# Kernel tuning notes

Measured on AMD Instinct MI355X. Metric: run time of the kernel, lower is better.

Reference implementation:

```python
import jax, jax.numpy as jnp
import numpy as np

N_NODES = 100000
N_EDGES = 1600000
EPS = 1e-5  # nn.BatchNorm1d default eps


def setup_inputs() -> dict:
    key = jax.random.key(0)
    ks = jax.random.split(key, 6)
    x = jax.random.normal(ks[0], (N_NODES, 11), dtype=jnp.float32)
    edge_index = jax.random.randint(ks[1], (2, N_EDGES), 0, N_NODES, dtype=jnp.int64)
    edge_weight = jax.random.uniform(ks[2], (N_EDGES,), dtype=jnp.float32)
    W1 = jax.random.normal(ks[3], (11, 64), dtype=jnp.float32) * 0.3
    b1 = jnp.zeros((64,), dtype=jnp.float32)
    gamma = jnp.ones((64,), dtype=jnp.float32)
    beta = jnp.zeros((64,), dtype=jnp.float32)
    W2 = jax.random.normal(ks[4], (64, 128), dtype=jnp.float32) * 0.125
    b2 = jnp.zeros((128,), dtype=jnp.float32)
    return {"x": x, "edge_index": edge_index, "edge_weight": edge_weight,
            "W1": W1, "b1": b1, "gamma": gamma, "beta": beta, "W2": W2, "b2": b2}


def _gcn_conv(x, row, col, w, W, b, n_nodes):
    """PyG GCNConv: h = x @ W; symmetric-norm aggregate at col; + bias.
    row/col/w already include self loops (weight 1.0)."""
    h = x @ W  # [N, F_out]
    deg = jax.ops.segment_sum(w, col, num_segments=n_nodes)  # [N]
    dinv = jnp.where(deg > 0, jax.lax.rsqrt(jnp.maximum(deg, 1e-12)), 0.0)
    norm = dinv[row] * w * dinv[col]  # [E+N]
    msg = h[row] * norm[:, None]  # gather + scale, [E+N, F_out]
    out = jax.ops.segment_sum(msg, col, num_segments=n_nodes)  # scatter-add
    return out + b


def _batch_norm(x, gamma, beta):
    # training-mode BatchNorm1d over node dimension, biased variance
    mean = jnp.mean(x, axis=0)
    var = jnp.mean(jnp.square(x - mean), axis=0)
    return (x - mean) * jax.lax.rsqrt(var + EPS) * gamma + beta


def reference(x, edge_index, edge_weight, W1, b1, gamma, beta, W2, b2):
    n = x.shape[0]
    loops = jnp.arange(n, dtype=edge_index.dtype)
    row = jnp.concatenate([edge_index[0], loops])
    col = jnp.concatenate([edge_index[1], loops])
    w = jnp.concatenate([edge_weight, jnp.ones((n,), dtype=edge_weight.dtype)])

    h = _gcn_conv(x, row, col, w, W1, b1, n)
    h = _batch_norm(h, gamma, beta)
    h = jax.nn.relu(h)
    # dropout is identity at inference (deterministic baseline)
    out = _gcn_conv(h, row, col, w, W2, b2, n)
    return out
```

## Files before the change

kernel.cpp:

```cpp
#include <hip/hip_runtime.h>

#define F0 11
#define F1 64
#define F2 128
#define TN2 128

#define CHUNKS 64
#define BPR 12544
#define WPR (BPR / 2)
#define NBKT (CHUNKS * 8 * 4)
#define NN1 64

__device__ __forceinline__ unsigned short f2bf(float v) {
  unsigned u = __float_as_uint(v);
  unsigned r = u + 0x7FFFu + ((u >> 16) & 1u);
  return (unsigned short)(r >> 16);
}
__device__ __forceinline__ float bf2f(unsigned short s) {
  return __uint_as_float(((unsigned)s) << 16);
}
__device__ __forceinline__ float bf2f_lo(unsigned v) { return __uint_as_float(v << 16); }
__device__ __forceinline__ float bf2f_hi(unsigned v) { return __uint_as_float(v & 0xFFFF0000u); }

__global__ void k_pad(const float* __restrict__ x, unsigned short* __restrict__ x16b, int n) {
  int i = blockIdx.x * blockDim.x + threadIdx.x;
  if (i >= n * 16) return;
  int r = i >> 4, f = i & 15;
  x16b[i] = (f < F0) ? f2bf(x[(size_t)r * F0 + f]) : (unsigned short)0;
}

__global__ __launch_bounds__(1024) void k_cnt8(const int* __restrict__ col,
                                               int* __restrict__ bcnt, int E, int CE) {
  __shared__ int scnt[16][8];
  int bid = blockIdx.x;
  int c = bid >> 2, q = bid & 3;
  int e0 = c * CE, e1 = min(E, e0 + CE);
  int S = (CE + 3) >> 2;
  int s0 = e0 + q * S, s1 = min(e1, s0 + S);
  int t = threadIdx.x, wv = t >> 6, lane = t & 63;
  int cr[8] = {0, 0, 0, 0, 0, 0, 0, 0};
  for (int e = s0 + t; e < s1; e += 1024) {
    int r = col[e] / BPR;
#pragma unroll
    for (int rr = 0; rr < 8; rr++) cr[rr] += (r == rr) ? 1 : 0;
  }
#pragma unroll
  for (int rr = 0; rr < 8; rr++) {
    int v = cr[rr];
#pragma unroll
    for (int d = 32; d > 0; d >>= 1) v += __shfl_down(v, d);
    if (lane == 0) scnt[wv][rr] = v;
  }
  __syncthreads();
  if (t < 8) {
    int s = 0;
    for (int i = 0; i < 16; i++) s += scnt[i][t];
    bcnt[(c * 8 + t) * 4 + q] = s;
  }
}

__global__ void k_scan8(const int* __restrict__ bcnt, int* __restrict__ boff) {
  __shared__ int s[1024];
  int t = threadIdx.x;
  int v0 = bcnt[2 * t], v1 = bcnt[2 * t + 1];
  int pv = v0 + v1;
  s[t] = pv;
  __syncthreads();
  for (int d = 1; d < 1024; d <<= 1) {
    int x = (t >= d) ? s[t - d] : 0;
    __syncthreads();
    s[t] += x;
    __syncthreads();
  }
  int ex = s[t] - pv;
  boff[2 * t] = ex;
  boff[2 * t + 1] = ex + v0;
  if (t == 1023) boff[2048] = s[1023];
}

__global__ __launch_bounds__(1024) void k_scatter(const int* __restrict__ col,
                                                  const int* __restrict__ row,
                                                  const float* __restrict__ w,
                                                  const int* __restrict__ boff,
                                                  unsigned short* __restrict__ bloc,
                                                  uint2* __restrict__ brw, int E, int CE) {
  __shared__ int cur[8];
  int bid = blockIdx.x;
  int c = bid >> 2, q = bid & 3;
  int t = threadIdx.x;
  if (t < 8) cur[t] = boff[(c * 8 + t) * 4 + q];
  __syncthreads();
  int e0 = c * CE, e1 = min(E, e0 + CE);
  int S = (CE + 3) >> 2;
  int s0 = e0 + q * S, s1 = min(e1, s0 + S);
  for (int e = s0 + t; e < s1; e += 1024) {
    int b = col[e];
    int r = b / BPR;
    int pos = atomicAdd(&cur[r], 1);
    bloc[pos] = (unsigned short)(b - r * BPR);
    brw[pos] = make_uint2((unsigned)row[e], __float_as_uint(w[e]));
  }
}

__global__ __launch_bounds__(1024) void k_hist2(const unsigned short* __restrict__ bloc,
                                                const int* __restrict__ boff,
                                                unsigned* __restrict__ partial, int ranges) {
  __shared__ unsigned lds[WPR];
  int r = blockIdx.x % ranges;
  int c = blockIdx.x / ranges;
  int t = threadIdx.x;
  for (int i = t; i < WPR; i += 1024) lds[i] = 0;
  __syncthreads();
  int s0 = boff[(c * 8 + r) * 4], s1 = boff[(c * 8 + r) * 4 + 4];
  for (int i = s0 + t; i < s1; i += 1024) {
    int local = bloc[i];
    atomicAdd(&lds[local >> 1], 1u << (16 * (local & 1)));
  }
  __syncthreads();
  unsigned* dst = partial + ((size_t)r * CHUNKS + c) * WPR;
  for (int i = t; i < WPR; i += 1024) dst[i] = lds[i];
}

__global__ void k_colprefix(const unsigned* __restrict__ partial,
                            unsigned short* __restrict__ rel,
                            int* __restrict__ cnt, int N, int npad) {
  int bin = blockIdx.x * blockDim.x + threadIdx.x;
  if (bin >= N) return;
  int r = bin / BPR, local = bin % BPR;
  int word = local >> 1, sh = 16 * (local & 1);
  const unsigned* p = partial + (size_t)r * CHUNKS * WPR + word;
  unsigned acc = 0;
  for (int c = 0; c < CHUNKS; c++) {
    unsigned v = (p[(size_t)c * WPR] >> sh) & 0xFFFFu;
    rel[(size_t)c * npad + bin] = (unsigned short)acc;
    acc += v;
  }
  cnt[bin] = (int)acc;
}

__global__ void k_scan1(const int* __restrict__ cnt, int* __restrict__ offs,
                        int* __restrict__ bsum, int n) {
  __shared__ int s[1024];
  int tid = threadIdx.x;
  int i = blockIdx.x * 1024 + tid;
  int v = (i < n) ? cnt[i] : 0;
  s[tid] = v;
  __syncthreads();
  for (int d = 1; d < 1024; d <<= 1) {
    int t = (tid >= d) ? s[tid - d] : 0;
    __syncthreads();
    s[tid] += t;
    __syncthreads();
  }
  if (i < n) offs[i] = s[tid] - v;
  if (tid == 1023) bsum[blockIdx.x] = s[1023];
}

__global__ void k_scan2(int* __restrict__ bsum, int nb) {
  __shared__ int s[256];
  __shared__ int carry;
  int t = threadIdx.x;
  if (t == 0) carry = 0;
  __syncthreads();
  for (int base = 0; base < nb; base += 256) {
    int v = (base + t < nb) ? bsum[base + t] : 0;
    s[t] = v;
    __syncthreads();
    for (int d = 1; d < 256; d <<= 1) {
      int x = (t >= d) ? s[t - d] : 0;
      __syncthreads();
      s[t] += x;
      __syncthreads();
    }
    int total = s[255];
    if (base + t < nb) bsum[base + t] = carry + s[t] - v;
    __syncthreads();
    if (t == 0) carry += total;
    __syncthreads();
  }
}

__global__ void k_scan3(int* __restrict__ offs, const int* __restrict__ bsum,
                        int n, int total) {
  int i = blockIdx.x * 1024 + threadIdx.x;
  if (i < n) offs[i] += bsum[blockIdx.x];
  if (i == 0) offs[n] = total;
}

__global__ __launch_bounds__(1024) void k_fill2(const unsigned short* __restrict__ bloc,
                                                const uint2* __restrict__ brw,
                                                const int* __restrict__ boff,
                                                const int* __restrict__ offs,
                                                const unsigned short* __restrict__ rel,
                                                uint2* __restrict__ csr8,
                                                int N, int npad, int ranges) {
  __shared__ unsigned cur[WPR];
  int r = blockIdx.x % ranges;
  int c = blockIdx.x / ranges;
  int lo = r * BPR;
  int hi = min(N, lo + BPR);
  int t = threadIdx.x;
  const unsigned* rsrc = (const unsigned*)(rel + (size_t)c * npad + lo);
  int nw = (hi - lo + 1) >> 1;
  for (int i = t; i < nw; i += 1024) cur[i] = rsrc[i];
  __syncthreads();
  int s0 = boff[(c * 8 + r) * 4], s1 = boff[(c * 8 + r) * 4 + 4];
  for (int i = s0 + t; i < s1; i += 1024) {
    int local = bloc[i];
    int sh = 16 * (local & 1);
    unsigned old = atomicAdd(&cur[local >> 1], 1u << sh);
    unsigned myrel = (old >> sh) & 0xFFFFu;
    int pos = offs[lo + local] + (int)myrel;
    uint2 b = brw[i];
    csr8[pos] = make_uint2(b.x | ((unsigned)local << 17), b.y);
  }
}

__global__ void k_deg2(const uint2* __restrict__ csr8, const int* __restrict__ offs,
                       float* __restrict__ dinv, int n) {
  int wid = (blockIdx.x * blockDim.x + threadIdx.x) >> 6;
  int lane = threadIdx.x & 63;
  if (wid >= n) return;
  int s = offs[wid], e = offs[wid + 1];
  float acc = 0.f;
  for (int k = s + lane; k < e; k += 64) acc += __uint_as_float(csr8[k].y);
#pragma unroll
  for (int d = 32; d > 0; d >>= 1) acc += __shfl_down(acc, d);
  if (lane == 0) dinv[wid] = rsqrtf(1.0f + acc);
}

__global__ void k_norm(uint2* __restrict__ csr8, const float* __restrict__ dinv, int E) {
  int i = blockIdx.x * blockDim.x + threadIdx.x;
  if (i >= E) return;
  uint2 v = csr8[i];
  csr8[i].y = __float_as_uint(dinv[v.x & 0x1FFFFu] * __uint_as_float(v.y));
}

__global__ __launch_bounds__(256) void k_agg1e(const unsigned short* __restrict__ x16b,
                                               const int* __restrict__ offs,
                                               const uint2* __restrict__ csr8,
                                               const float* __restrict__ dinv,
                                               const float* __restrict__ W1,
                                               const float* __restrict__ b1,
                                               unsigned short* __restrict__ h,
                                               float2* __restrict__ pbn, int N) {
  __shared__ float Ws[F0 * F1];
  __shared__ float bs[F1];
  __shared__ float sacc[NN1 * 16];
  __shared__ unsigned short sx[NN1 * 16];
  __shared__ float sdinv[NN1];
  __shared__ float sS[4][64], sQ[4][64];
  int t = threadIdx.x;
  int bid = blockIdx.x;
  int n0 = bid * NN1;
  int nn = min(NN1, N - n0);
  int lbase = n0 - (n0 / BPR) * BPR;
  for (int i = t; i < F0 * F1; i += 256) Ws[i] = W1[i];
  if (t < F1) bs[t] = b1[t];
  ((uint2*)sx)[t] = ((const uint2*)(x16b + (size_t)n0 * 16))[t];
  if (t < NN1) sdinv[t] = (t < nn) ? dinv[n0 + t] : 0.f;
  for (int i = t; i < NN1 * 16; i += 256) sacc[i] = 0.f;
  __syncthreads();
  int ebase = offs[n0], eend = offs[n0 + nn];
  int slot = t >> 4, f = t & 15;
  int nsub = (eend - ebase + 15) >> 4;
  int gs = ebase + slot * nsub;
  int ge = min(eend, gs + nsub);
  float sum = 0.f;
  int cid = -1;
  int e = gs;
  for (; e + 4 <= ge; e += 4) {
    uint2 v0 = csr8[e], v1 = csr8[e + 1], v2 = csr8[e + 2], v3 = csr8[e + 3];
    int i0 = (int)(v0.x >> 17) - lbase, i1 = (int)(v1.x >> 17) - lbase;
    int i2 = (int)(v2.x >> 17) - lbase, i3 = (int)(v3.x >> 17) - lbase;
    float c0 = __uint_as_float(v0.y) * bf2f(x16b[(size_t)(v0.x & 0x1FFFFu) * 16 + f]);
    float c1 = __uint_as_float(v1.y) * bf2f(x16b[(size_t)(v1.x & 0x1FFFFu) * 16 + f]);
    float c2 = __uint_as_float(v2.y) * bf2f(x16b[(size_t)(v2.x & 0x1FFFFu) * 16 + f]);
    float c3 = __uint_as_float(v3.y) * bf2f(x16b[(size_t)(v3.x & 0x1FFFFu) * 16 + f]);
    bool sm;
    sm = (i0 == cid); if (!sm && cid >= 0) atomicAdd(&sacc[cid * 16 + f], sum);
    sum = sm ? sum + c0 : c0; cid = i0;
    sm = (i1 == cid); if (!sm) atomicAdd(&sacc[cid * 16 + f], sum);
    sum = sm ? sum + c1 : c1; cid = i1;
    sm = (i2 == cid); if (!sm) atomicAdd(&sacc[cid * 16 + f], sum);
    sum = sm ? sum + c2 : c2; cid = i2;
    sm = (i3 == cid); if (!sm) atomicAdd(&sacc[cid * 16 + f], sum);
    sum = sm ? sum + c3 : c3; cid = i3;
  }
  for (; e < ge; e++) {
    uint2 v0 = csr8[e];
    int i0 = (int)(v0.x >> 17) - lbase;
    float c0 = __uint_as_float(v0.y) * bf2f(x16b[(size_t)(v0.x & 0x1FFFFu) * 16 + f]);
    bool sm = (i0 == cid);
    if (!sm && cid >= 0) atomicAdd(&sacc[cid * 16 + f], sum);
    sum = sm ? sum + c0 : c0; cid = i0;
  }
  if (cid >= 0) atomicAdd(&sacc[cid * 16 + f], sum);
  __syncthreads();
  for (int i = t; i < NN1 * 16; i += 256) {
    float di = sdinv[i >> 4];
    sacc[i] = di * (sacc[i] + di * bf2f(sx[i]));
  }
  __syncthreads();
  int ff = t & 63, wv = t >> 6;
  float S = 0.f, Q = 0.f;
  for (int i = 0; i < 16; i++) {
    int nd = wv + 4 * i;
    if (nd < nn) {
      float o = bs[ff];
#pragma unroll
      for (int k = 0; k < F0; k++) o += sacc[nd * 16 + k] * Ws[k * F1 + ff];
      h[(size_t)(n0 + nd) * F1 + ff] = f2bf(o);
      S += o; Q += o * o;
    }
  }
  sS[wv][ff] = S; sQ[wv][ff] = Q;
  __syncthreads();
  if (t < 64)
    pbn[(size_t)bid * 64 + t] =
        make_float2(sS[0][t] + sS[1][t] + sS[2][t] + sS[3][t],
                    sQ[0][t] + sQ[1][t] + sQ[2][t] + sQ[3][t]);
}

__global__ void k_bn_mid(const float2* __restrict__ pbn, float2* __restrict__ pbn2, int nrows) {
  __shared__ float sS[4][64], sQ[4][64];
  int t = threadIdx.x;
  int f = t & 63, g = t >> 6;
  int rpb = (nrows + 63) / 64;
  int b0 = blockIdx.x * rpb;
  int bend = min(nrows, b0 + rpb);
  float S = 0.f, Q = 0.f;
  for (int b = b0 + g; b < bend; b += 4) {
    float2 v = pbn[(size_t)b * 64 + f];
    S += v.x; Q += v.y;
  }
  sS[g][f] = S; sQ[g][f] = Q;
  __syncthreads();
  if (t < 64)
    pbn2[(size_t)blockIdx.x * 64 + t] =
        make_float2(sS[0][t] + sS[1][t] + sS[2][t] + sS[3][t],
                    sQ[0][t] + sQ[1][t] + sQ[2][t] + sQ[3][t]);
}

__global__ void k_bn_final(const float2* __restrict__ pbn2, const float* __restrict__ gamma,
                           const float* __restrict__ beta, float* __restrict__ scalef,
                           float* __restrict__ shiftf, int n) {
  __shared__ double sS[4][64], sQ[4][64];
  int t = threadIdx.x;
  int f = t & 63, g = t >> 6;
  double S = 0.0, Q = 0.0;
  for (int b = g; b < 64; b += 4) {
    float2 v = pbn2[(size_t)b * 64 + f];
    S += v.x; Q += v.y;
  }
  sS[g][f] = S; sQ[g][f] = Q;
  __syncthreads();
  if (t < 64) {
    double SS = sS[0][t] + sS[1][t] + sS[2][t] + sS[3][t];
    double QQ = sQ[0][t] + sQ[1][t] + sQ[2][t] + sQ[3][t];
    double mean = SS / (double)n;
    double var = QQ / (double)n - mean * mean;
    if (var < 0.0) var = 0.0;
    float scale = gamma[t] * (float)(1.0 / sqrt(var + 1e-5));
    scalef[t] = scale;
    shiftf[t] = beta[t] - (float)mean * scale;
  }
}

__global__ void k_hn(const unsigned short* __restrict__ h, const float* __restrict__ scalef,
                     const float* __restrict__ shiftf, unsigned short* __restrict__ hn,
                     int total4) {
  __shared__ float ssc[64], ssf[64];
  int t = threadIdx.x;
  if (t < 64) { ssc[t] = scalef[t]; ssf[t] = shiftf[t]; }
  __syncthreads();
  int idx = blockIdx.x * blockDim.x + t;
  int stride = gridDim.x * blockDim.x;
  const unsigned long long* hp = (const unsigned long long*)h;
  unsigned long long* hnp = (unsigned long long*)hn;
  for (int i = idx; i < total4; i += stride) {
    unsigned long long vv = hp[i];
    int f0 = (i * 4) & 63;
    float a = fmaxf(fmaf(bf2f_lo((unsigned)vv), ssc[f0 + 0], ssf[f0 + 0]), 0.f);
    float b = fmaxf(fmaf(bf2f_hi((unsigned)vv), ssc[f0 + 1], ssf[f0 + 1]), 0.f);
    float c = fmaxf(fmaf(bf2f_lo((unsigned)(vv >> 32)), ssc[f0 + 2], ssf[f0 + 2]), 0.f);
    float d = fmaxf(fmaf(bf2f_hi((unsigned)(vv >> 32)), ssc[f0 + 3], ssf[f0 + 3]), 0.f);
    hnp[i] = (unsigned long long)f2bf(a) | ((unsigned long long)f2bf(b) << 16) |
             ((unsigned long long)f2bf(c) << 32) | ((unsigned long long)f2bf(d) << 48);
  }
}

__global__ __launch_bounds__(256) void k_agg2e(const unsigned short* __restrict__ hn,
                                               const int* __restrict__ offs,
                                               const uint2* __restrict__ csr8,
                                               const float* __restrict__ dinv,
                                               float* __restrict__ agg2, int N) {
  __shared__ float sacc[NN1 * F1];
  __shared__ float sdinv[NN1];
  int t = threadIdx.x;
  int bid = blockIdx.x;
  int n0 = bid * NN1;
  int nn = min(NN1, N - n0);
  int lbase = n0 - (n0 / BPR) * BPR;
  int lane = t & 63, wv = t >> 6;
  if (t < NN1) sdinv[t] = (t < nn) ? dinv[n0 + t] : 0.f;
  for (int i = t; i < NN1 * F1; i += 256) sacc[i] = 0.f;
  __syncthreads();
  int ebase = offs[n0], eend = offs[n0 + nn];
  int nsub = (eend - ebase + 3) >> 2;
  int gs = ebase + wv * nsub;
  int ge = min(eend, gs + nsub);
  float sum = 0.f;
  int cid = -1;
  int e = gs;
  for (; e + 8 <= ge; e += 8) {
    uint2 v[8];
#pragma unroll
    for (int j = 0; j < 8; j++) v[j] = csr8[e + j];
    float c[8];
    int idx[8];
#pragma unroll
    for (int j = 0; j < 8; j++) {
      idx[j] = (int)(v[j].x >> 17) - lbase;
      c[j] = __uint_as_float(v[j].y) *
             bf2f(hn[(size_t)(v[j].x & 0x1FFFFu) * F1 + lane]);
    }
#pragma unroll
    for (int j = 0; j < 8; j++) {
      bool sm = (idx[j] == cid);
      if (!sm && cid >= 0) atomicAdd(&sacc[cid * F1 + lane], sum);
      sum = sm ? sum + c[j] : c[j];
      cid = idx[j];
    }
  }
  for (; e < ge; e++) {
    uint2 v0 = csr8[e];
    int i0 = (int)(v0.x >> 17) - lbase;
    float c0 = __uint_as_float(v0.y) * bf2f(hn[(size_t)(v0.x & 0x1FFFFu) * F1 + lane]);
    bool sm = (i0 == cid);
    if (!sm && cid >= 0) atomicAdd(&sacc[cid * F1 + lane], sum);
    sum = sm ? sum + c0 : c0;
    cid = i0;
  }
  if (cid >= 0) atomicAdd(&sacc[cid * F1 + lane], sum);
  __syncthreads();
  for (int i = 0; i < 16; i++) {
    int nd = wv + 4 * i;
    if (nd < nn) {
      float di = sdinv[nd];
      float self = bf2f(hn[(size_t)(n0 + nd) * F1 + lane]);
      agg2[(size_t)(n0 + nd) * F1 + lane] = di * (sacc[nd * F1 + lane] + di * self);
    }
  }
}

__global__ __launch_bounds__(256) void k_gemm2(const float* __restrict__ agg2,
                                               const float* __restrict__ W2,
                                               const float* __restrict__ b2,
                                               float* __restrict__ out, int n) {
  __shared__ float Ws[F1 * F2];
  __shared__ float As[F1][TN2];
  int t = threadIdx.x;
  for (int i = t; i < F1 * F2 / 4; i += 256) ((float4*)Ws)[i] = ((const float4*)W2)[i];
  int nb = blockIdx.x * TN2;
  int node = t & 127;
  int kh = (t >> 7) * 32;
  int gnode = nb + node;
  if (gnode < n) {
    const float4* src = (const float4*)(agg2 + (size_t)gnode * F1 + kh);
#pragma unroll
    for (int j = 0; j < 8; j++) {
      float4 v = src[j];
      As[kh + j * 4 + 0][node] = v.x;
      As[kh + j * 4 + 1][node] = v.y;
      As[kh + j * 4 + 2][node] = v.z;
      As[kh + j * 4 + 3][node] = v.w;
    }
  } else {
#pragma unroll
    for (int j = 0; j < 8; j++) {
      As[kh + j * 4 + 0][node] = 0.f;
      As[kh + j * 4 + 1][node] = 0.f;
      As[kh + j * 4 + 2][node] = 0.f;
      As[kh + j * 4 + 3][node] = 0.f;
    }
  }
  __syncthreads();

  int f0 = (t & 15) * 8;
  int n0 = (t >> 4) * 8;
  float acc[8][8];
  float bv[8];
#pragma unroll
  for (int j = 0; j < 8; j++) bv[j] = b2[f0 + j];
#pragma unroll
  for (int i = 0; i < 8; i++)
#pragma unroll
    for (int j = 0; j < 8; j++) acc[i][j] = bv[j];

#pragma unroll 4
  for (int k = 0; k < F1; k++) {
    float4 a0 = *(const float4*)&As[k][n0];
    float4 a1 = *(const float4*)&As[k][n0 + 4];
    float4 w0 = *(const float4*)&Ws[k * F2 + f0];
    float4 w1 = *(const float4*)&Ws[k * F2 + f0 + 4];
    float a[8] = {a0.x, a0.y, a0.z, a0.w, a1.x, a1.y, a1.z, a1.w};
    float w[8] = {w0.x, w0.y, w0.z, w0.w, w1.x, w1.y, w1.z, w1.w};
#pragma unroll
    for (int i = 0; i < 8; i++)
#pragma unroll
      for (int j = 0; j < 8; j++) acc[i][j] += a[i] * w[j];
  }

#pragma unroll
  for (int i = 0; i < 8; i++) {
    int gi = nb + n0 + i;
    if (gi < n) {
      float4 o0 = {acc[i][0], acc[i][1], acc[i][2], acc[i][3]};
      float4 o1 = {acc[i][4], acc[i][5], acc[i][6], acc[i][7]};
      *(float4*)&out[(size_t)gi * F2 + f0] = o0;
      *(float4*)&out[(size_t)gi * F2 + f0 + 4] = o1;
    }
  }
}

extern "C" void kernel_launch(void* const* d_in, const int* in_sizes, int n_in,
                              void* d_out, int out_size, void* d_ws, size_t ws_size,
                              hipStream_t stream) {
  const float* x     = (const float*)d_in[0];
  const int*   ei    = (const int*)d_in[1];
  const float* ew    = (const float*)d_in[2];
  const float* W1    = (const float*)d_in[3];
  const float* b1    = (const float*)d_in[4];
  const float* gamma = (const float*)d_in[5];
  const float* beta  = (const float*)d_in[6];
  const float* W2    = (const float*)d_in[7];
  const float* b2    = (const float*)d_in[8];
  float* out = (float*)d_out;

  int N = in_sizes[0] / F0;
  int E = in_sizes[1] / 2;
  const int* row = ei;
  const int* col = ei + E;
  if (N <= 0) return;

  int CE = (E + CHUNKS - 1) / CHUNKS;
  int RANGES = (N + BPR - 1) / BPR;
  int npad = RANGES * BPR;
  int NBLK = (N + NN1 - 1) / NN1;

  char* p = (char*)d_ws;
  auto alloc = [&](size_t bytes) -> void* {
    void* r = (void*)p;
    p += (bytes + 255) & ~(size_t)255;
    return r;
  };
  size_t partial_bytes = ((size_t)RANGES * CHUNKS * WPR * 4 + 255) & ~(size_t)255;
  size_t rel_bytes     = (size_t)CHUNKS * npad * 2;
  size_t h_bytes       = (size_t)N * F1 * 2;
  size_t region_bytes  = partial_bytes + rel_bytes;
  if (h_bytes > region_bytes) region_bytes = h_bytes;

  float*          dinv    = (float*)alloc((size_t)N * 4);
  int*            cnt     = (int*)alloc((size_t)N * 4);
  int*            offs    = (int*)alloc((size_t)(N + 1) * 4);
  int             NB      = (N + 1023) / 1024;
  int*            bsum    = (int*)alloc((size_t)NB * 4);
  uint2*          csr8    = (uint2*)alloc((size_t)E * 8);
  char*           region  = (char*)alloc(region_bytes);
  unsigned*       partial = (unsigned*)region;
  unsigned short* rel     = (unsigned short*)(region + partial_bytes);
  unsigned short* h       = (unsigned short*)region;
  unsigned short* x16b    = (unsigned short*)alloc((size_t)N * 16 * 2);
  unsigned short* hn      = (unsigned short*)alloc((size_t)N * F1 * 2);
  float*          agg2    = (float*)alloc((size_t)N * F1 * 4);
  float2*         pbn     = (float2*)alloc((size_t)NBLK * 64 * 8);
  float2*         pbn2    = (float2*)alloc((size_t)64 * 64 * 8);
  float*          scalef  = (float*)alloc(64 * 4);
  float*          shiftf  = (float*)alloc(64 * 4);
  int*            bcnt    = (int*)alloc((size_t)NBKT * 4);
  int*            boff    = (int*)alloc((size_t)(NBKT + 1) * 4);
  size_t bloc_bytes = (((size_t)E * 2) + 255) & ~(size_t)255;
  unsigned short* bloc = (unsigned short*)agg2;
  uint2*          brw  = (uint2*)((char*)agg2 + bloc_bytes);
  (void)ws_size; (void)n_in; (void)out_size;

  int bW  = (N + 3) / 4;
  int bG2 = (N + TN2 - 1) / TN2;
  int gRC = CHUNKS * RANGES;

  k_pad<<<(N * 16 + 255) / 256, 256, 0, stream>>>(x, x16b, N);
  k_cnt8<<<CHUNKS * 4, 1024, 0, stream>>>(col, bcnt, E, CE);
  k_scan8<<<1, 1024, 0, stream>>>(bcnt, boff);
  k_scatter<<<CHUNKS * 4, 1024, 0, stream>>>(col, row, ew, boff, bloc, brw, E, CE);
  k_hist2<<<gRC, 1024, 0, stream>>>(bloc, boff, partial, RANGES);
  k_colprefix<<<(N + 255) / 256, 256, 0, stream>>>(partial, rel, cnt, N, npad);
  k_scan1<<<NB, 1024, 0, stream>>>(cnt, offs, bsum, N);
  k_scan2<<<1, 256, 0, stream>>>(bsum, NB);
  k_scan3<<<NB, 1024, 0, stream>>>(offs, bsum, N, E);
  k_fill2<<<gRC, 1024, 0, stream>>>(bloc, brw, boff, offs, rel, csr8, N, npad, RANGES);
  k_deg2<<<bW, 256, 0, stream>>>(csr8, offs, dinv, N);
  k_norm<<<(E + 255) / 256, 256, 0, stream>>>(csr8, dinv, E);
  k_agg1e<<<NBLK, 256, 0, stream>>>(x16b, offs, csr8, dinv, W1, b1, h, pbn, N);
  k_bn_mid<<<64, 256, 0, stream>>>(pbn, pbn2, NBLK);
  k_bn_final<<<1, 256, 0, stream>>>(pbn2, gamma, beta, scalef, shiftf, N);
  k_hn<<<2048, 256, 0, stream>>>(h, scalef, shiftf, hn, N * F1 / 4);
  k_agg2e<<<NBLK, 256, 0, stream>>>(hn, offs, csr8, dinv, agg2, N);
  k_gemm2<<<bG2, 256, 0, stream>>>(agg2, W2, b2, out, N);
}
```

Baseline: 246.1 us.

## Replace edge-split LDS-atomic second aggregation with wavefront-per-node pull gather

The second-layer aggregation no longer splits each 64-node block's edge range across four waves that combine partial sums with shared-memory atomics. Instead, each 64-lane wavefront owns one destination node. It stages that node's CSR entries in LDS, then gathers neighbour rows with eight independent accumulators before writing the normalised result. This removes the LDS atomics, the shared accumulator tile and the segment-boundary logic. In exchange, work per wave follows node degree, and partial batches of eight edges are padded with zero-weight loads of row 0.

```diff
diff --git a/kernel.cpp b/kernel.cpp
--- a/kernel.cpp
+++ b/kernel.cpp
@@ -390,68 +390,52 @@
   }
 }
 
-__global__ __launch_bounds__(256) void k_agg2e(const unsigned short* __restrict__ hn,
-                                               const int* __restrict__ offs,
-                                               const uint2* __restrict__ csr8,
-                                               const float* __restrict__ dinv,
-                                               float* __restrict__ agg2, int N) {
-  __shared__ float sacc[NN1 * F1];
-  __shared__ float sdinv[NN1];
-  int t = threadIdx.x;
-  int bid = blockIdx.x;
-  int n0 = bid * NN1;
-  int nn = min(NN1, N - n0);
-  int lbase = n0 - (n0 / BPR) * BPR;
-  int lane = t & 63, wv = t >> 6;
-  if (t < NN1) sdinv[t] = (t < nn) ? dinv[n0 + t] : 0.f;
-  for (int i = t; i < NN1 * F1; i += 256) sacc[i] = 0.f;
-  __syncthreads();
-  int ebase = offs[n0], eend = offs[n0 + nn];
-  int nsub = (eend - ebase + 3) >> 2;
-  int gs = ebase + wv * nsub;
-  int ge = min(eend, gs + nsub);
-  float sum = 0.f;
-  int cid = -1;
-  int e = gs;
-  for (; e + 8 <= ge; e += 8) {
-    uint2 v[8];
-#pragma unroll
-    for (int j = 0; j < 8; j++) v[j] = csr8[e + j];
-    float c[8];
-    int idx[8];
-#pragma unroll
-    for (int j = 0; j < 8; j++) {
-      idx[j] = (int)(v[j].x >> 17) - lbase;
-      c[j] = __uint_as_float(v[j].y) *
-             bf2f(hn[(size_t)(v[j].x & 0x1FFFFu) * F1 + lane]);
-    }
-#pragma unroll
-    for (int j = 0; j < 8; j++) {
-      bool sm = (idx[j] == cid);
-      if (!sm && cid >= 0) atomicAdd(&sacc[cid * F1 + lane], sum);
-      sum = sm ? sum + c[j] : c[j];
-      cid = idx[j];
-    }
-  }
-  for (; e < ge; e++) {
-    uint2 v0 = csr8[e];
-    int i0 = (int)(v0.x >> 17) - lbase;
-    float c0 = __uint_as_float(v0.y) * bf2f(hn[(size_t)(v0.x & 0x1FFFFu) * F1 + lane]);
-    bool sm = (i0 == cid);
-    if (!sm && cid >= 0) atomicAdd(&sacc[cid * F1 + lane], sum);
-    sum = sm ? sum + c0 : c0;
-    cid = i0;
-  }
-  if (cid >= 0) atomicAdd(&sacc[cid * F1 + lane], sum);
-  __syncthreads();
-  for (int i = 0; i < 16; i++) {
-    int nd = wv + 4 * i;
-    if (nd < nn) {
-      float di = sdinv[nd];
-      float self = bf2f(hn[(size_t)(n0 + nd) * F1 + lane]);
-      agg2[(size_t)(n0 + nd) * F1 + lane] = di * (sacc[nd * F1 + lane] + di * self);
-    }
-  }
+__global__ void k_agg2(const unsigned short* __restrict__ hn, const int* __restrict__ offs,
+                       const uint2* __restrict__ csr8, const float* __restrict__ dinv,
+                       float* __restrict__ agg2, int n) {
+  __shared__ unsigned s_soff[4][64];
+  __shared__ float    s_nrm[4][64];
+  int t = threadIdx.x;
+  int wv = t >> 6;
+  int lane = t & 63;
+  int wid = (blockIdx.x * blockDim.x + t) >> 6;
+  if (wid >= n) return;
+  float di = dinv[wid];
+  float a0 = di * bf2f(hn[(size_t)wid * F1 + lane]);
+  float a1 = 0.f, a2 = 0.f, a3 = 0.f, a4 = 0.f, a5 = 0.f, a6 = 0.f, a7 = 0.f;
+  int s = offs[wid], e = offs[wid + 1];
+  for (int base = s; base < e; base += 64) {
+    int m = e - base; if (m > 64) m = 64;
+    if (lane < m) {
+      uint2 v = csr8[base + lane];
+      s_soff[wv][lane] = (v.x & 0x1FFFFu) * 64u;
+      s_nrm[wv][lane] = __uint_as_float(v.y);
+    } else {
+      s_soff[wv][lane] = 0u;
+      s_nrm[wv][lane] = 0.f;
+    }
+    int mp = (m + 7) & ~7;
+    for (int j = 0; j < mp; j += 8) {
+      unsigned o0 = s_soff[wv][j + 0], o1 = s_soff[wv][j + 1];
+      unsigned o2 = s_soff[wv][j + 2], o3 = s_soff[wv][j + 3];
+      unsigned o4 = s_soff[wv][j + 4], o5 = s_soff[wv][j + 5];
+      unsigned o6 = s_soff[wv][j + 6], o7 = s_soff[wv][j + 7];
+      float m0 = s_nrm[wv][j + 0], m1 = s_nrm[wv][j + 1];
+      float m2 = s_nrm[wv][j + 2], m3 = s_nrm[wv][j + 3];
+      float m4 = s_nrm[wv][j + 4], m5 = s_nrm[wv][j + 5];
+      float m6 = s_nrm[wv][j + 6], m7 = s_nrm[wv][j + 7];
+      a0 += m0 * bf2f(hn[(size_t)o0 + lane]);
+      a1 += m1 * bf2f(hn[(size_t)o1 + lane]);
+      a2 += m2 * bf2f(hn[(size_t)o2 + lane]);
+      a3 += m3 * bf2f(hn[(size_t)o3 + lane]);
+      a4 += m4 * bf2f(hn[(size_t)o4 + lane]);
+      a5 += m5 * bf2f(hn[(size_t)o5 + lane]);
+      a6 += m6 * bf2f(hn[(size_t)o6 + lane]);
+      a7 += m7 * bf2f(hn[(size_t)o7 + lane]);
+    }
+  }
+  agg2[(size_t)wid * F1 + lane] =
+      di * (((a0 + a1) + (a2 + a3)) + ((a4 + a5) + (a6 + a7)));
 }
 
 __global__ __launch_bounds__(256) void k_gemm2(const float* __restrict__ agg2,
@@ -605,6 +589,6 @@
   k_bn_mid<<<64, 256, 0, stream>>>(pbn, pbn2, NBLK);
   k_bn_final<<<1, 256, 0, stream>>>(pbn2, gamma, beta, scalef, shiftf, N);
   k_hn<<<2048, 256, 0, stream>>>(h, scalef, shiftf, hn, N * F1 / 4);
-  k_agg2e<<<NBLK, 256, 0, stream>>>(hn, offs, csr8, dinv, agg2, N);
+  k_agg2<<<bW, 256, 0, stream>>>(hn, offs, csr8, dinv, agg2, N);
   k_gemm2<<<bG2, 256, 0, stream>>>(agg2, W2, b2, out, N);
 }
```

Measured after the change: 214.1 us. -13.0%, faster.
